# Optimization experiments

Hardware: AMD Instinct MI355X
Metric: run time of the kernel (lower is better)

Reference implementation:

```python
import jax, jax.numpy as jnp
import numpy as np

C, K, B, H, W = 96, 7, 32, 112, 112
EPS = 1e-5


def setup_inputs() -> dict:
    key = jax.random.key(0)
    k1, k2, k3 = jax.random.split(key, 3)
    local_hk = jax.random.normal(k1, (C, 1, K, K), dtype=jnp.float32)  # depthwise kernel [C,1,k,k]
    x = jax.random.normal(k2, (B, C, H, W), dtype=jnp.float32)
    # kaiming_normal_ for a 1x1 conv: std = sqrt(2 / fan_in), fan_in = C
    w_mix = jax.random.normal(k3, (C, C), dtype=jnp.float32) * np.float32(np.sqrt(2.0 / C))
    b_mix = jnp.zeros((C,), dtype=jnp.float32)  # bias filled with 0.0
    return {"local_hk": local_hk, "x": x, "w_mix": w_mix, "b_mix": b_mix}


def reference(local_hk, x, w_mix, b_mix):
    groups = local_hk.shape[0]
    pad = (local_hk.shape[-1] - 1) // 2
    # dynamic depthwise conv2d (groups == C, C_in/groups == 1)
    feat = jax.lax.conv_general_dilated(
        x, local_hk,
        window_strides=(1, 1),
        padding=((pad, pad), (pad, pad)),
        feature_group_count=groups,
        dimension_numbers=("NCHW", "OIHW", "NCHW"),
    )
    # 1x1 channel mixer (Linear2d): out[b,o,h,w] = sum_c feat[b,c,h,w] * w[o,c] + bias[o]
    feat = jnp.einsum("bchw,oc->bohw", feat, w_mix) + b_mix[None, :, None, None]
    # BatchNorm2d(affine=False, track_running_stats=False): batch stats, biased variance
    mean = jnp.mean(feat, axis=(0, 2, 3), keepdims=True)
    var = jnp.var(feat, axis=(0, 2, 3), keepdims=True)
    feat = (feat - mean) * jax.lax.rsqrt(var + EPS)
    # exact (erf-based) GELU, matching torch.nn.GELU default
    return jax.nn.gelu(feat, approximate=False)
```

## Files before the change

### kernel.cpp

```cpp
#include <hip/hip_runtime.h>
#include <cstdint>
#include <cstddef>

#define CC   96
#define BB   32
#define HHn  112
#define WWn  112
#define HWn  (HHn*WWn)
#define NPIX (BB*HWn)
#define EPSf 1e-5f

typedef __attribute__((ext_vector_type(8))) short bf16x8;
typedef __attribute__((ext_vector_type(4))) float f32x4;

__device__ inline unsigned short f2bf(float f) {
  unsigned u = __float_as_uint(f);
  return (unsigned short)((u + 0x7FFFu + ((u >> 16) & 1u)) >> 16);
}
__device__ inline float bf2f(unsigned short h) {
  return __uint_as_float(((unsigned)h) << 16);
}

__global__ __launch_bounds__(256) void k_prep(const float* __restrict__ w,
                                              unsigned short* __restrict__ wbf) {
  int i = blockIdx.x * 256 + threadIdx.x;
  if (i < CC * CC) wbf[i] = f2bf(w[i]);
}

__global__ __launch_bounds__(512, 6) void k_conv(const float* __restrict__ x,
                                                 const float* __restrict__ hk,
                                                 unsigned short* __restrict__ feat) {
  __shared__ float lplane[HWn];

  int tid = threadIdx.x;
  int plane = __builtin_amdgcn_readfirstlane(blockIdx.x);
  int c = plane % CC;
  const float* xp = x + (long)plane * HWn;
  unsigned short* fp = feat + (long)plane * HWn;

#pragma unroll
  for (int it = 0; it < 6; ++it) {
    float4 v = *(const float4*)(xp + it * 2048 + tid * 4);
    *(float4*)(&lplane[it * 2048 + tid * 4]) = v;
  }
  if (tid < 64) {
    float4 v = *(const float4*)(xp + 12288 + tid * 4);
    *(float4*)(&lplane[12288 + tid * 4]) = v;
  }

  float wk[49];
  const float* kc = hk + c * 49;
#pragma unroll
  for (int i = 0; i < 49; ++i)
    wk[i] = __uint_as_float(__builtin_amdgcn_readfirstlane(__float_as_uint(kc[i])));

  int q = tid / 28;
  int s = tid % 28;
  int cb = s * 4;
  int qb = q * 7;
  bool aok0 = (s > 0);
  bool cok0 = (s < 27);
  int offA = aok0 ? cb - 4 : 0;
  int offC = cok0 ? cb + 4 : cb;

  float acc[7][4];
#pragma unroll
  for (int i = 0; i < 7; ++i)
#pragma unroll
    for (int j = 0; j < 4; ++j) acc[i][j] = 0.f;

  __syncthreads();

  if (tid < 448) {
#pragma unroll
    for (int rr = 0; rr < 13; ++rr) {
      int r = qb + rr - 3;
      bool vok = ((unsigned)r < (unsigned)HHn);
      int rc = r < 0 ? 0 : (r > HHn - 1 ? HHn - 1 : r);
      const float* row = &lplane[rc * WWn];
      float4 A  = *(const float4*)(row + offA);
      float4 Bv = *(const float4*)(row + cb);
      float4 Cv = *(const float4*)(row + offC);
      bool aok = vok && aok0;
      bool cok = vok && cok0;
      float win[10];
      win[0] = aok ? A.y : 0.f;
      win[1] = aok ? A.z : 0.f;
      win[2] = aok ? A.w : 0.f;
      win[3] = vok ? Bv.x : 0.f;
      win[4] = vok ? Bv.y : 0.f;
      win[5] = vok ? Bv.z : 0.f;
      win[6] = vok ? Bv.w : 0.f;
      win[7] = cok ? Cv.x : 0.f;
      win[8] = cok ? Cv.y : 0.f;
      win[9] = cok ? Cv.z : 0.f;

#pragma unroll
      for (int kh = 0; kh < 7; ++kh) {
        if (rr >= kh && rr - kh <= 6) {
          const int slot = rr - kh;
#pragma unroll
          for (int kw = 0; kw < 7; ++kw) {
            float wv = wk[kh * 7 + kw];
#pragma unroll
            for (int j = 0; j < 4; ++j)
              acc[slot][j] = fmaf(win[j + kw], wv, acc[slot][j]);
          }
        }
      }

      if (rr >= 6) {
        const int slot = rr - 6;
        unsigned short* orow = fp + (qb + slot) * WWn + cb;
        uint2 pk;
        pk.x = (unsigned)f2bf(acc[slot][0]) | ((unsigned)f2bf(acc[slot][1]) << 16);
        pk.y = (unsigned)f2bf(acc[slot][2]) | ((unsigned)f2bf(acc[slot][3]) << 16);
        *(uint2*)orow = pk;
      }
    }
  }
}

__global__ __launch_bounds__(256, 2) void k_mix(const unsigned short* __restrict__ feat,
                                                const unsigned short* __restrict__ wbf,
                                                unsigned short* __restrict__ mixed,
                                                float* __restrict__ ssum,
                                                float* __restrict__ ssq) {
  __shared__ unsigned short flds[256 * 128];
  __shared__ float lsum[CC], lsq[CC];

  int tid = threadIdx.x;
  int bid = blockIdx.x;
  int b = bid / 49, tile = bid % 49;
  int p0 = tile * 256;

  if (tid < CC) { lsum[tid] = 0.f; lsq[tid] = 0.f; }

  const unsigned short* fb = feat + (long)b * CC * HWn + p0;
  int u   = (tid >> 3) & 7;
  int v   = tid & 7;
  int wv  = tid >> 6;
  int pgl = wv * 8 + v;

  bf16x8 vals[12];
#pragma unroll
  for (int s = 0; s < 12; ++s) {
    int c = s * 8 + u;
    vals[s] = *(const bf16x8*)(fb + (long)c * HWn + pgl * 8);
  }
#pragma unroll
  for (int s = 0; s < 12; ++s) {
#pragma unroll
    for (int e = 0; e < 8; ++e) {
      int pl = pgl * 8 + e;
      int kp = (pl ^ (pl >> 3)) & 7;
      flds[pl * 128 + ((s ^ kp) << 3) + u] = (unsigned short)vals[s][e];
    }
  }

  int l = tid & 63;
  int lm = l & 15, lg = l >> 4;
  bf16x8 a[6][3];
#pragma unroll
  for (int mt = 0; mt < 6; ++mt)
#pragma unroll
    for (int kk = 0; kk < 3; ++kk)
      a[mt][kk] = *(const bf16x8*)(wbf + (mt * 16 + lm) * CC + kk * 32 + lg * 8);

  __syncthreads();

  f32x4 acc[6][4];
#pragma unroll
  for (int mt = 0; mt < 6; ++mt)
#pragma unroll
    for (int j = 0; j < 4; ++j) acc[mt][j] = (f32x4){0.f, 0.f, 0.f, 0.f};

#pragma unroll
  for (int j = 0; j < 4; ++j) {
    int pl = (wv * 4 + j) * 16 + lm;
    int kp = (pl ^ (pl >> 3)) & 7;
#pragma unroll
    for (int kk = 0; kk < 3; ++kk) {
      bf16x8 bfrag = *(const bf16x8*)(&flds[pl * 128 + (((kk * 4 + lg) ^ kp) << 3)]);
#pragma unroll
      for (int mt = 0; mt < 6; ++mt)
        acc[mt][j] = __builtin_amdgcn_mfma_f32_16x16x32_bf16(a[mt][kk], bfrag, acc[mt][j], 0, 0, 0);
    }
  }

  __syncthreads();

#pragma unroll
  for (int mt = 0; mt < 6; ++mt) {
#pragma unroll
    for (int r = 0; r < 4; ++r) {
      int o = mt * 16 + lg * 4 + r;
      float s = 0.f, q = 0.f;
#pragma unroll
      for (int j = 0; j < 4; ++j) {
        unsigned short h = f2bf(acc[mt][j][r]);
        float vv = bf2f(h);
        int px = (wv * 4 + j) * 16 + lm;
        flds[o * 256 + (px ^ (lg << 4))] = h;
        s += vv; q += vv * vv;
      }
      s += __shfl_xor(s, 1); q += __shfl_xor(q, 1);
      s += __shfl_xor(s, 2); q += __shfl_xor(q, 2);
      s += __shfl_xor(s, 4); q += __shfl_xor(q, 4);
      s += __shfl_xor(s, 8); q += __shfl_xor(q, 8);
      if (lm == 0) { atomicAdd(&lsum[o], s); atomicAdd(&lsq[o], q); }
    }
  }
  __syncthreads();

  unsigned short* mbase = mixed + (long)b * CC * HWn + p0;
  int o2 = tid >> 5;
  int pxg = tid & 31;
#pragma unroll
  for (int i = 0; i < 12; ++i) {
    int o = i * 8 + o2;
    int key = (o >> 2) & 3;
    uint4 vv = *(const uint4*)(&flds[o * 256 + ((pxg * 8) ^ (key << 4))]);
    *(uint4*)(mbase + (long)o * HWn + pxg * 8) = vv;
  }

  if (tid < CC) atomicAdd(&ssum[tid], lsum[tid]);
  else if (tid < 2 * CC) atomicAdd(&ssq[tid - CC], lsq[tid - CC]);
}

__global__ void k_finalize(const float* __restrict__ ssum,
                           const float* __restrict__ ssq,
                           float* __restrict__ meanv,
                           float* __restrict__ rstdv) {
  int o = threadIdx.x;
  if (o < CC) {
    float m = ssum[o] * (1.0f / NPIX);
    float v = ssq[o] * (1.0f / NPIX) - m * m;
    meanv[o] = m;
    rstdv[o] = 1.0f / sqrtf(v + EPSf);
  }
}

__global__ __launch_bounds__(256) void k_bngelu(const unsigned short* __restrict__ mixed,
                                                const float* __restrict__ meanv,
                                                const float* __restrict__ rstdv,
                                                float* __restrict__ out) {
  long e = ((long)blockIdx.x * 256 + threadIdx.x) * 8;
  int o = (int)((e / HWn) % CC);
  float m = meanv[o], r = rstdv[o];
  bf16x8 v = *(const bf16x8*)(mixed + e);
  float4 g0, g1;
  float z;
  z = (bf2f((unsigned short)v[0]) - m) * r; g0.x = 0.5f * z * (1.0f + erff(z * 0.70710678f));
  z = (bf2f((unsigned short)v[1]) - m) * r; g0.y = 0.5f * z * (1.0f + erff(z * 0.70710678f));
  z = (bf2f((unsigned short)v[2]) - m) * r; g0.z = 0.5f * z * (1.0f + erff(z * 0.70710678f));
  z = (bf2f((unsigned short)v[3]) - m) * r; g0.w = 0.5f * z * (1.0f + erff(z * 0.70710678f));
  z = (bf2f((unsigned short)v[4]) - m) * r; g1.x = 0.5f * z * (1.0f + erff(z * 0.70710678f));
  z = (bf2f((unsigned short)v[5]) - m) * r; g1.y = 0.5f * z * (1.0f + erff(z * 0.70710678f));
  z = (bf2f((unsigned short)v[6]) - m) * r; g1.z = 0.5f * z * (1.0f + erff(z * 0.70710678f));
  z = (bf2f((unsigned short)v[7]) - m) * r; g1.w = 0.5f * z * (1.0f + erff(z * 0.70710678f));
  *(float4*)(out + e)     = g0;
  *(float4*)(out + e + 4) = g1;
}

extern "C" void kernel_launch(void* const* d_in, const int* in_sizes, int n_in,
                              void* d_out, int out_size, void* d_ws, size_t ws_size,
                              hipStream_t stream) {
  const float* hk   = (const float*)d_in[0];
  const float* x    = (const float*)d_in[1];
  const float* wmix = (const float*)d_in[2];
  const float* bmix = (const float*)d_in[3];
  (void)bmix;
  float* out = (float*)d_out;

  char* ws = (char*)d_ws;
  float* stats = (float*)ws;
  unsigned short* wbf     = (unsigned short*)(ws + 2048);
  unsigned short* featbf  = (unsigned short*)(ws + 32768);
  unsigned short* mixedbf = (unsigned short*)(ws + 32768 + 77070336);

  hipMemsetAsync(stats, 0, 768, stream);

  k_prep<<<36, 256, 0, stream>>>(wmix, wbf);
  k_conv<<<3072, 512, 0, stream>>>(x, hk, featbf);
  k_mix<<<1568, 256, 0, stream>>>(featbf, wbf, mixedbf, stats, stats + 96);
  k_finalize<<<1, 128, 0, stream>>>(stats, stats + 96, stats + 192, stats + 288);
  k_bngelu<<<18816, 256, 0, stream>>>(mixedbf, stats + 192, stats + 288, out);
}
```

Baseline: 187.4 us.

## Recompute channel mix in BN-GELU pass and read conv input from global

```diff
diff --git a/kernel.cpp b/kernel.cpp
--- a/kernel.cpp
+++ b/kernel.cpp
@@ -27,37 +27,29 @@
   if (i < CC * CC) wbf[i] = f2bf(w[i]);
 }
 
-__global__ __launch_bounds__(512, 6) void k_conv(const float* __restrict__ x,
+__global__ __launch_bounds__(256, 6) void k_conv(const float* __restrict__ x,
                                                  const float* __restrict__ hk,
                                                  unsigned short* __restrict__ feat) {
-  __shared__ float lplane[HWn];
-
   int tid = threadIdx.x;
-  int plane = __builtin_amdgcn_readfirstlane(blockIdx.x);
+  int bid = blockIdx.x;
+  int plane = __builtin_amdgcn_readfirstlane(bid >> 1);
+  int half  = __builtin_amdgcn_readfirstlane(bid & 1);
   int c = plane % CC;
   const float* xp = x + (long)plane * HWn;
   unsigned short* fp = feat + (long)plane * HWn;
 
-#pragma unroll
-  for (int it = 0; it < 6; ++it) {
-    float4 v = *(const float4*)(xp + it * 2048 + tid * 4);
-    *(float4*)(&lplane[it * 2048 + tid * 4]) = v;
-  }
-  if (tid < 64) {
-    float4 v = *(const float4*)(xp + 12288 + tid * 4);
-    *(float4*)(&lplane[12288 + tid * 4]) = v;
-  }
-
   float wk[49];
   const float* kc = hk + c * 49;
 #pragma unroll
   for (int i = 0; i < 49; ++i)
     wk[i] = __uint_as_float(__builtin_amdgcn_readfirstlane(__float_as_uint(kc[i])));
+
+  if (tid >= 224) return;
 
   int q = tid / 28;
   int s = tid % 28;
   int cb = s * 4;
-  int qb = q * 7;
+  int qb = half * 56 + q * 7;
   bool aok0 = (s > 0);
   bool cok0 = (s < 27);
   int offA = aok0 ? cb - 4 : 0;
@@ -69,63 +61,58 @@
 #pragma unroll
     for (int j = 0; j < 4; ++j) acc[i][j] = 0.f;
 
-  __syncthreads();
-
-  if (tid < 448) {
-#pragma unroll
-    for (int rr = 0; rr < 13; ++rr) {
-      int r = qb + rr - 3;
-      bool vok = ((unsigned)r < (unsigned)HHn);
-      int rc = r < 0 ? 0 : (r > HHn - 1 ? HHn - 1 : r);
-      const float* row = &lplane[rc * WWn];
-      float4 A  = *(const float4*)(row + offA);
-      float4 Bv = *(const float4*)(row + cb);
-      float4 Cv = *(const float4*)(row + offC);
-      bool aok = vok && aok0;
-      bool cok = vok && cok0;
-      float win[10];
-      win[0] = aok ? A.y : 0.f;
-      win[1] = aok ? A.z : 0.f;
-      win[2] = aok ? A.w : 0.f;
-      win[3] = vok ? Bv.x : 0.f;
-      win[4] = vok ? Bv.y : 0.f;
-      win[5] = vok ? Bv.z : 0.f;
-      win[6] = vok ? Bv.w : 0.f;
-      win[7] = cok ? Cv.x : 0.f;
-      win[8] = cok ? Cv.y : 0.f;
-      win[9] = cok ? Cv.z : 0.f;
-
-#pragma unroll
-      for (int kh = 0; kh < 7; ++kh) {
-        if (rr >= kh && rr - kh <= 6) {
-          const int slot = rr - kh;
-#pragma unroll
-          for (int kw = 0; kw < 7; ++kw) {
-            float wv = wk[kh * 7 + kw];
-#pragma unroll
-            for (int j = 0; j < 4; ++j)
-              acc[slot][j] = fmaf(win[j + kw], wv, acc[slot][j]);
-          }
+#pragma unroll
+  for (int rr = 0; rr < 13; ++rr) {
+    int r = qb + rr - 3;
+    bool vok = ((unsigned)r < (unsigned)HHn);
+    int rc = r < 0 ? 0 : (r > HHn - 1 ? HHn - 1 : r);
+    const float* row = xp + rc * WWn;
+    float4 A  = *(const float4*)(row + offA);
+    float4 Bv = *(const float4*)(row + cb);
+    float4 Cv = *(const float4*)(row + offC);
+    bool aok = vok && aok0;
+    bool cok = vok && cok0;
+    float win[10];
+    win[0] = aok ? A.y : 0.f;
+    win[1] = aok ? A.z : 0.f;
+    win[2] = aok ? A.w : 0.f;
+    win[3] = vok ? Bv.x : 0.f;
+    win[4] = vok ? Bv.y : 0.f;
+    win[5] = vok ? Bv.z : 0.f;
+    win[6] = vok ? Bv.w : 0.f;
+    win[7] = cok ? Cv.x : 0.f;
+    win[8] = cok ? Cv.y : 0.f;
+    win[9] = cok ? Cv.z : 0.f;
+
+#pragma unroll
+    for (int kh = 0; kh < 7; ++kh) {
+      if (rr >= kh && rr - kh <= 6) {
+        const int slot = rr - kh;
+#pragma unroll
+        for (int kw = 0; kw < 7; ++kw) {
+          float wv = wk[kh * 7 + kw];
+#pragma unroll
+          for (int j = 0; j < 4; ++j)
+            acc[slot][j] = fmaf(win[j + kw], wv, acc[slot][j]);
         }
       }
-
-      if (rr >= 6) {
-        const int slot = rr - 6;
-        unsigned short* orow = fp + (qb + slot) * WWn + cb;
-        uint2 pk;
-        pk.x = (unsigned)f2bf(acc[slot][0]) | ((unsigned)f2bf(acc[slot][1]) << 16);
-        pk.y = (unsigned)f2bf(acc[slot][2]) | ((unsigned)f2bf(acc[slot][3]) << 16);
-        *(uint2*)orow = pk;
-      }
-    }
-  }
-}
-
-__global__ __launch_bounds__(256, 2) void k_mix(const unsigned short* __restrict__ feat,
-                                                const unsigned short* __restrict__ wbf,
-                                                unsigned short* __restrict__ mixed,
-                                                float* __restrict__ ssum,
-                                                float* __restrict__ ssq) {
+    }
+
+    if (rr >= 6) {
+      const int slot = rr - 6;
+      unsigned short* orow = fp + (qb + slot) * WWn + cb;
+      uint2 pk;
+      pk.x = (unsigned)f2bf(acc[slot][0]) | ((unsigned)f2bf(acc[slot][1]) << 16);
+      pk.y = (unsigned)f2bf(acc[slot][2]) | ((unsigned)f2bf(acc[slot][3]) << 16);
+      *(uint2*)orow = pk;
+    }
+  }
+}
+
+__global__ __launch_bounds__(256, 2) void k_stats(const unsigned short* __restrict__ feat,
+                                                  const unsigned short* __restrict__ wbf,
+                                                  float* __restrict__ ssum,
+                                                  float* __restrict__ ssq) {
   __shared__ unsigned short flds[256 * 128];
   __shared__ float lsum[CC], lsq[CC];
 
@@ -188,8 +175,6 @@
     }
   }
 
-  __syncthreads();
-
 #pragma unroll
   for (int mt = 0; mt < 6; ++mt) {
 #pragma unroll
@@ -198,10 +183,7 @@
       float s = 0.f, q = 0.f;
 #pragma unroll
       for (int j = 0; j < 4; ++j) {
-        unsigned short h = f2bf(acc[mt][j][r]);
-        float vv = bf2f(h);
-        int px = (wv * 4 + j) * 16 + lm;
-        flds[o * 256 + (px ^ (lg << 4))] = h;
+        float vv = acc[mt][j][r];
         s += vv; q += vv * vv;
       }
       s += __shfl_xor(s, 1); q += __shfl_xor(q, 1);
@@ -212,17 +194,6 @@
     }
   }
   __syncthreads();
-
-  unsigned short* mbase = mixed + (long)b * CC * HWn + p0;
-  int o2 = tid >> 5;
-  int pxg = tid & 31;
-#pragma unroll
-  for (int i = 0; i < 12; ++i) {
-    int o = i * 8 + o2;
-    int key = (o >> 2) & 3;
-    uint4 vv = *(const uint4*)(&flds[o * 256 + ((pxg * 8) ^ (key << 4))]);
-    *(uint4*)(mbase + (long)o * HWn + pxg * 8) = vv;
-  }
 
   if (tid < CC) atomicAdd(&ssum[tid], lsum[tid]);
   else if (tid < 2 * CC) atomicAdd(&ssq[tid - CC], lsq[tid - CC]);
@@ -241,26 +212,88 @@
   }
 }
 
-__global__ __launch_bounds__(256) void k_bngelu(const unsigned short* __restrict__ mixed,
-                                                const float* __restrict__ meanv,
-                                                const float* __restrict__ rstdv,
-                                                float* __restrict__ out) {
-  long e = ((long)blockIdx.x * 256 + threadIdx.x) * 8;
-  int o = (int)((e / HWn) % CC);
-  float m = meanv[o], r = rstdv[o];
-  bf16x8 v = *(const bf16x8*)(mixed + e);
-  float4 g0, g1;
-  float z;
-  z = (bf2f((unsigned short)v[0]) - m) * r; g0.x = 0.5f * z * (1.0f + erff(z * 0.70710678f));
-  z = (bf2f((unsigned short)v[1]) - m) * r; g0.y = 0.5f * z * (1.0f + erff(z * 0.70710678f));
-  z = (bf2f((unsigned short)v[2]) - m) * r; g0.z = 0.5f * z * (1.0f + erff(z * 0.70710678f));
-  z = (bf2f((unsigned short)v[3]) - m) * r; g0.w = 0.5f * z * (1.0f + erff(z * 0.70710678f));
-  z = (bf2f((unsigned short)v[4]) - m) * r; g1.x = 0.5f * z * (1.0f + erff(z * 0.70710678f));
-  z = (bf2f((unsigned short)v[5]) - m) * r; g1.y = 0.5f * z * (1.0f + erff(z * 0.70710678f));
-  z = (bf2f((unsigned short)v[6]) - m) * r; g1.z = 0.5f * z * (1.0f + erff(z * 0.70710678f));
-  z = (bf2f((unsigned short)v[7]) - m) * r; g1.w = 0.5f * z * (1.0f + erff(z * 0.70710678f));
-  *(float4*)(out + e)     = g0;
-  *(float4*)(out + e + 4) = g1;
+__global__ __launch_bounds__(256, 2) void k_bngelu(const unsigned short* __restrict__ feat,
+                                                   const unsigned short* __restrict__ wbf,
+                                                   const float* __restrict__ meanv,
+                                                   const float* __restrict__ rstdv,
+                                                   float* __restrict__ out) {
+  __shared__ unsigned short flds[256 * 128];
+  __shared__ float smean[CC], srstd[CC];
+
+  int tid = threadIdx.x;
+  int bid = blockIdx.x;
+  int b = bid / 49, tile = bid % 49;
+  int p0 = tile * 256;
+
+  if (tid < CC) { smean[tid] = meanv[tid]; srstd[tid] = rstdv[tid]; }
+
+  const unsigned short* fb = feat + (long)b * CC * HWn + p0;
+  int u   = (tid >> 3) & 7;
+  int v   = tid & 7;
+  int wv  = tid >> 6;
+  int pgl = wv * 8 + v;
+
+  bf16x8 vals[12];
+#pragma unroll
+  for (int s = 0; s < 12; ++s) {
+    int c = s * 8 + u;
+    vals[s] = *(const bf16x8*)(fb + (long)c * HWn + pgl * 8);
+  }
+#pragma unroll
+  for (int s = 0; s < 12; ++s) {
+#pragma unroll
+    for (int e = 0; e < 8; ++e) {
+      int pl = pgl * 8 + e;
+      int kp = (pl ^ (pl >> 3)) & 7;
+      flds[pl * 128 + ((s ^ kp) << 3) + u] = (unsigned short)vals[s][e];
+    }
+  }
+
+  int l = tid & 63;
+  int lm = l & 15, lg = l >> 4;
+  bf16x8 a[6][3];
+#pragma unroll
+  for (int mt = 0; mt < 6; ++mt)
+#pragma unroll
+    for (int kk = 0; kk < 3; ++kk)
+      a[mt][kk] = *(const bf16x8*)(wbf + (mt * 16 + lm) * CC + kk * 32 + lg * 8);
+
+  __syncthreads();
+
+  f32x4 acc[6][4];
+#pragma unroll
+  for (int mt = 0; mt < 6; ++mt)
+#pragma unroll
+    for (int j = 0; j < 4; ++j) acc[mt][j] = (f32x4){0.f, 0.f, 0.f, 0.f};
+
+#pragma unroll
+  for (int j = 0; j < 4; ++j) {
+    int pl = (wv * 4 + j) * 16 + lm;
+    int kp = (pl ^ (pl >> 3)) & 7;
+#pragma unroll
+    for (int kk = 0; kk < 3; ++kk) {
+      bf16x8 bfrag = *(const bf16x8*)(&flds[pl * 128 + (((kk * 4 + lg) ^ kp) << 3)]);
+#pragma unroll
+      for (int mt = 0; mt < 6; ++mt)
+        acc[mt][j] = __builtin_amdgcn_mfma_f32_16x16x32_bf16(a[mt][kk], bfrag, acc[mt][j], 0, 0, 0);
+    }
+  }
+
+  float* ob = out + (long)b * CC * HWn + p0;
+#pragma unroll
+  for (int mt = 0; mt < 6; ++mt) {
+#pragma unroll
+    for (int r = 0; r < 4; ++r) {
+      int o = mt * 16 + lg * 4 + r;
+      float m = smean[o], rs = srstd[o];
+      float* orow = ob + (long)o * HWn + lm;
+#pragma unroll
+      for (int j = 0; j < 4; ++j) {
+        float z = (acc[mt][j][r] - m) * rs;
+        orow[(wv * 4 + j) * 16] = 0.5f * z * (1.0f + erff(z * 0.70710678f));
+      }
+    }
+  }
 }
 
 extern "C" void kernel_launch(void* const* d_in, const int* in_sizes, int n_in,
@@ -275,15 +308,14 @@
 
   char* ws = (char*)d_ws;
   float* stats = (float*)ws;
-  unsigned short* wbf     = (unsigned short*)(ws + 2048);
-  unsigned short* featbf  = (unsigned short*)(ws + 32768);
-  unsigned short* mixedbf = (unsigned short*)(ws + 32768 + 77070336);
+  unsigned short* wbf    = (unsigned short*)(ws + 2048);
+  unsigned short* featbf = (unsigned short*)(ws + 32768);
 
   hipMemsetAsync(stats, 0, 768, stream);
 
   k_prep<<<36, 256, 0, stream>>>(wmix, wbf);
-  k_conv<<<3072, 512, 0, stream>>>(x, hk, featbf);
-  k_mix<<<1568, 256, 0, stream>>>(featbf, wbf, mixedbf, stats, stats + 96);
+  k_conv<<<6144, 256, 0, stream>>>(x, hk, featbf);
+  k_stats<<<1568, 256, 0, stream>>>(featbf, wbf, stats, stats + 96);
   k_finalize<<<1, 128, 0, stream>>>(stats, stats + 96, stats + 192, stats + 288);
-  k_bngelu<<<18816, 256, 0, stream>>>(mixedbf, stats + 192, stats + 288, out);
-}
+  k_bngelu<<<1568, 256, 0, stream>>>(featbf, wbf, stats + 192, stats + 288, out);
+}
```

New measurement: 246.8 us. 31.7% more time.
